# Kernel optimization log

Measured on AMD Instinct MI355X. Metric: run time of the kernel, lower is better.

Reference implementation:

```python
import jax, jax.numpy as jnp
import numpy as np

N_NODES = 100000
N_EDGES = 1600000
N_REL = 2
IN_CH, HID_CH, OUT_CH = 128, 128, 64


def setup_inputs() -> dict:
    key = jax.random.key(0)
    ks = jax.random.split(key, 8)
    x = jax.random.normal(ks[0], (N_NODES, IN_CH), dtype=jnp.float32)
    edge_index = jax.random.randint(ks[1], (2, N_EDGES), 0, N_NODES, dtype=jnp.int64)
    edge_type = jax.random.randint(ks[2], (N_EDGES,), 0, N_REL, dtype=jnp.int64)
    s1 = 1.0 / np.sqrt(IN_CH)
    s2 = 1.0 / np.sqrt(HID_CH)
    W1_rel = jax.random.normal(ks[3], (N_REL, IN_CH, HID_CH), dtype=jnp.float32) * s1
    W1_root = jax.random.normal(ks[4], (IN_CH, HID_CH), dtype=jnp.float32) * s1
    b1 = jnp.zeros((HID_CH,), dtype=jnp.float32)
    W2_rel = jax.random.normal(ks[5], (N_REL, HID_CH, OUT_CH), dtype=jnp.float32) * s2
    W2_root = jax.random.normal(ks[6], (HID_CH, OUT_CH), dtype=jnp.float32) * s2
    b2 = jnp.zeros((OUT_CH,), dtype=jnp.float32)
    return {"x": x, "edge_index": edge_index, "edge_type": edge_type,
            "W1_rel": W1_rel, "W1_root": W1_root, "b1": b1,
            "W2_rel": W2_rel, "W2_root": W2_root, "b2": b2}


def rgcn_conv(x, edge_index, edge_type, W_rel, W_root, b):
    """Relational graph conv: root transform + per-relation gather/matmul/scatter-mean."""
    src, dst = edge_index[0], edge_index[1]
    N = x.shape[0]
    out = x @ W_root + b  # self/root term
    x_src = x[src]  # [E, in] gather once, reused across relations
    for r in range(W_rel.shape[0]):  # N_REL is small and fixed
        mask = (edge_type == r)
        msg = jnp.where(mask[:, None], x_src, 0.0) @ W_rel[r]  # [E, out]
        agg = jax.ops.segment_sum(msg, dst, num_segments=N)  # [N, out]
        cnt = jax.ops.segment_sum(mask.astype(x.dtype), dst, num_segments=N)
        out = out + agg / jnp.maximum(cnt, 1.0)[:, None]  # mean aggregation
    return out


def l2_normalize(x, eps=1e-12):
    nrm = jnp.sqrt(jnp.sum(x * x, axis=1, keepdims=True))
    return x / jnp.maximum(nrm, eps)


def reference(x, edge_index, edge_type, W1_rel, W1_root, b1, W2_rel, W2_root, b2):
    h = jax.nn.relu(rgcn_conv(x, edge_index, edge_type, W1_rel, W1_root, b1))
    out = rgcn_conv(h, edge_index, edge_type, W2_rel, W2_root, b2)
    return l2_normalize(out)
```

## Files before the change

kernel.cpp:

```cpp
#include <hip/hip_runtime.h>
#include <hip/hip_bf16.h>


typedef unsigned int uint;
typedef unsigned short ushort;
typedef __attribute__((ext_vector_type(8))) short short8;
typedef __attribute__((ext_vector_type(16))) float floatx16;
typedef __attribute__((ext_vector_type(2))) float f32x2;
typedef __attribute__((ext_vector_type(4))) float f32x4;
typedef __attribute__((ext_vector_type(4))) uint u32x4;

#define IN_CH  128
#define OUT_CH 64
#define SCAN_CHUNK 2048
#define EPB 8192
#define KPB 512
#define MAXBK 400

__device__ __forceinline__ ushort f2bf(float f) {
    uint u = __float_as_uint(f);
    u += 0x7FFF + ((u >> 16) & 1);
    return (ushort)(u >> 16);
}
__device__ __forceinline__ float bflo(uint u) { return __uint_as_float(u << 16); }
__device__ __forceinline__ float bfhi(uint u) { return __uint_as_float(u & 0xFFFF0000u); }


__global__ void k_scan_a(const int* __restrict__ deg, int* __restrict__ offs,
                         int* __restrict__ bsums, int n) {
    __shared__ int sdata[256];
    int b = blockIdx.x, t = threadIdx.x;
    int base = b * SCAN_CHUNK + t * 8;
    int v[8];
    int sum = 0;
#pragma unroll
    for (int i = 0; i < 8; i++) {
        int idx = base + i;
        int x = (idx < n) ? deg[idx] : 0;
        v[i] = sum;
        sum += x;
    }
    sdata[t] = sum;
    __syncthreads();
    for (int ofs = 1; ofs < 256; ofs <<= 1) {
        int val = sdata[t];
        int add = (t >= ofs) ? sdata[t - ofs] : 0;
        __syncthreads();
        sdata[t] = val + add;
        __syncthreads();
    }
    int texcl = (t == 0) ? 0 : sdata[t - 1];
    if (t == 255) bsums[b] = sdata[255];
#pragma unroll
    for (int i = 0; i < 8; i++) {
        int idx = base + i;
        if (idx < n) offs[idx] = texcl + v[i];
    }
}

__global__ void k_scan_b(int* __restrict__ bsums, int* __restrict__ offs, int nb, int n) {
    int t = threadIdx.x;
    if (nb <= 64) {
        int v = (t < nb) ? bsums[t] : 0;
        int s = v;
#pragma unroll
        for (int d = 1; d < 64; d <<= 1) {
            int u = __shfl_up(s, d, 64);
            if (t >= d) s += u;
        }
        if (t < nb) bsums[t] = s - v;
        if (t == 63) offs[n] = s;
    } else if (t == 0) {
        int run = 0;
        for (int b = 0; b < nb; b++) {
            int x = bsums[b];
            bsums[b] = run;
            run += x;
        }
        offs[n] = run;
    }
}

__global__ void k_part(const int* __restrict__ src, const int* __restrict__ dst,
                       const int* __restrict__ et, const int* __restrict__ basebb,
                       const int* __restrict__ bsums,
                       uint* __restrict__ stage, int E, int NBK, int NBLK) {
    __shared__ int cnt[MAXBK];
    __shared__ int basel[MAXBK];
    int tid = threadIdx.x, blk = blockIdx.x;
    for (int b = tid; b < NBK; b += 256) {
        cnt[b] = 0;
        int i = b * NBLK + blk;
        basel[b] = basebb[i] + bsums[i >> 11];
    }
    __syncthreads();
    int base = blk * EPB;
#pragma unroll 4
    for (int i = 0; i < EPB / 256; i++) {
        int e = base + i * 256 + tid;
        if (e < E) {
            int s = src[e];
            int key = 2 * dst[e] + et[e];
            int bk = key >> 9;
            int r = atomicAdd(&cnt[bk], 1);
            stage[basel[bk] + r] = ((uint)(key & 511) << 23) | (uint)s;
        }
    }
}

__global__ void k_fine(const uint* __restrict__ stage, const int* __restrict__ basebb,
                       const int* __restrict__ bsums,
                       int* __restrict__ offs, int* __restrict__ esrc,
                       int E, int NBK, int NBLK) {
    __shared__ int kcnt[KPB];
    __shared__ int kcur[KPB];
    __shared__ int ssum[256];
    int tid = threadIdx.x, b = blockIdx.x;
    int i0 = b * NBLK;
    int start = basebb[i0] + bsums[i0 >> 11];
    int endB = E;
    if (b != NBK - 1) {
        int i1 = (b + 1) * NBLK;
        endB = basebb[i1] + bsums[i1 >> 11];
    }
    int size = endB - start;

    kcnt[tid] = 0;
    kcnt[tid + 256] = 0;
    __syncthreads();
    for (int i = tid; i < size; i += 256)
        atomicAdd(&kcnt[stage[start + i] >> 23], 1);
    __syncthreads();
    int v0 = kcnt[2 * tid], v1 = kcnt[2 * tid + 1];
    ssum[tid] = v0 + v1;
    __syncthreads();
    for (int ofs = 1; ofs < 256; ofs <<= 1) {
        int val = ssum[tid];
        int add = (tid >= ofs) ? ssum[tid - ofs] : 0;
        __syncthreads();
        ssum[tid] = val + add;
        __syncthreads();
    }
    int texcl = (tid == 0) ? 0 : ssum[tid - 1];
    kcur[2 * tid] = texcl;
    kcur[2 * tid + 1] = texcl + v0;
    offs[(b << 9) + 2 * tid] = start + texcl + v0;
    offs[(b << 9) + 2 * tid + 1] = start + texcl + v0 + v1;
    __syncthreads();
    for (int i = tid; i < size; i += 256) {
        uint p = stage[start + i];
        int r = atomicAdd(&kcur[p >> 23], 1);
        esrc[start + r] = (int)(p & 0x7FFFFFu);
    }
}


__device__ __forceinline__ uint4 pack8(const ushort* o) {
    uint4 v;
    v.x = (uint)o[0] | ((uint)o[1] << 16);
    v.y = (uint)o[2] | ((uint)o[3] << 16);
    v.z = (uint)o[4] | ((uint)o[5] << 16);
    v.w = (uint)o[6] | ((uint)o[7] << 16);
    return v;
}

__global__ void k_pre(const int* __restrict__ dst, const int* __restrict__ et,
                      int* __restrict__ cntblk, int E, int NBK, int NBLK,
                      const float* __restrict__ x, uint4* __restrict__ xb, int n8,
                      const float* __restrict__ W1root, const float* __restrict__ W1rel,
                      const float* __restrict__ W2root, const float* __restrict__ W2rel,
                      uint4* __restrict__ Bpk1, uint4* __restrict__ Bpk2,
                      uint* __restrict__ xzero, uint* __restrict__ t2zero) {
    __shared__ int cnt[MAXBK];
    int tid = threadIdx.x;
    if ((int)blockIdx.x < NBLK) {
        int blk = blockIdx.x;
        for (int b = tid; b < NBK; b += 256) cnt[b] = 0;
        __syncthreads();
        int base = blk * EPB;
#pragma unroll 4
        for (int i = 0; i < EPB / 256; i++) {
            int e = base + i * 256 + tid;
            if (e < E) {
                int key = 2 * dst[e] + et[e];
                atomicAdd(&cnt[key >> 9], 1);
            }
        }
        __syncthreads();
        for (int b = tid; b < NBK; b += 256) cntblk[b * NBLK + blk] = cnt[b];
        return;
    }
    int bid = blockIdx.x - NBLK;
    if (bid < 40) {
        if (bid == 0) {
            if (tid < 64) xzero[tid] = 0;
            if (tid < 96) t2zero[tid] = 0;
        }
        int idx = bid * 256 + tid;
        ushort o[8];
        if (idx < 6144) {
            int id = idx;
            int ct = id >> 11;
            int c = id & 2047;
            int gn = c >> 9, s = (c >> 6) & 7, h = (c >> 5) & 1, n = c & 31;
            int k0 = s * 16 + h * 8;
            int col = gn * 32 + n;
            const float* W = (ct == 0) ? W1root : (W1rel + (size_t)(ct - 1) * 16384);
#pragma unroll
            for (int j = 0; j < 8; j++) o[j] = f2bf(W[(k0 + j) * 128 + col]);
            Bpk1[id] = pack8(o);
        } else {
            int id = idx - 6144;
            int ct = id >> 11;
            int c = id & 2047;
            int gn = c >> 9, s = (c >> 6) & 7, h = (c >> 5) & 1, n = c & 31;
            int k0 = s * 16 + h * 8;
            int colg = ct * 128 + gn * 32 + n;
#pragma unroll
            for (int j = 0; j < 8; j++) {
                float f = 0.f;
                if (colg < 64)       f = W2root[(k0 + j) * 64 + colg];
                else if (colg < 128) f = W2rel[(k0 + j) * 64 + (colg - 64)];
                else if (colg < 192) f = W2rel[8192 + (k0 + j) * 64 + (colg - 128)];
                o[j] = f2bf(f);
            }
            Bpk2[id] = pack8(o);
        }
    } else {
        int i = (bid - 40) * 256 + tid;
        if (i >= n8) return;
        const f32x4* xp = (const f32x4*)x;
        f32x4 f0 = __builtin_nontemporal_load(&xp[(size_t)i * 2]);
        f32x4 f1 = __builtin_nontemporal_load(&xp[(size_t)i * 2 + 1]);
        uint4 o;
        o.x = (uint)f2bf(f0.x) | ((uint)f2bf(f0.y) << 16);
        o.y = (uint)f2bf(f0.z) | ((uint)f2bf(f0.w) << 16);
        o.z = (uint)f2bf(f1.x) | ((uint)f2bf(f1.y) << 16);
        o.w = (uint)f2bf(f1.z) | ((uint)f2bf(f1.w) << 16);
        xb[i] = o;
    }
}


__global__ __launch_bounds__(256)
void k_agg(const int* __restrict__ offs, const int* __restrict__ esrc,
           const uint4* __restrict__ xb4, uint4* __restrict__ S4, int N) {
    int wid = (int)((blockIdx.x * 256L + threadIdx.x) >> 5);
    int l = threadIdx.x & 31;
    if (wid >= N) return;
    int q = l >> 4, c = l & 15;

    int beg0 = (wid == 0) ? 0 : offs[2 * wid - 1];
    int end0 = offs[2 * wid], end1 = offs[2 * wid + 1];

    uint4 o = make_uint4(0, 0, 0, 0);
#pragma unroll
    for (int r = 0; r < 2; r++) {
        int beg = r ? end0 : beg0;
        int end = r ? end1 : end0;
        f32x2 a0 = {0.f, 0.f}, a1 = {0.f, 0.f}, a2 = {0.f, 0.f}, a3 = {0.f, 0.f};
        for (int c0 = beg; c0 < end; c0 += 32) {
            int myid = (c0 + l < end) ? __builtin_nontemporal_load(&esrc[c0 + l]) : N;
            int m = min(32, end - c0);
            for (int eb = 0; eb < m; eb += 4) {
#pragma unroll
                for (int j = 0; j < 2; j++) {
                    int id = __shfl(myid, eb + 2 * j + q, 32);
                    uint4 v = xb4[(uint)id * 16u + (uint)c];
                    a0 += (f32x2){bflo(v.x), bfhi(v.x)};
                    a1 += (f32x2){bflo(v.y), bfhi(v.y)};
                    a2 += (f32x2){bflo(v.z), bfhi(v.z)};
                    a3 += (f32x2){bflo(v.w), bfhi(v.w)};
                }
            }
        }
        a0.x += __shfl_xor(a0.x, 16, 32); a0.y += __shfl_xor(a0.y, 16, 32);
        a1.x += __shfl_xor(a1.x, 16, 32); a1.y += __shfl_xor(a1.y, 16, 32);
        a2.x += __shfl_xor(a2.x, 16, 32); a2.y += __shfl_xor(a2.y, 16, 32);
        a3.x += __shfl_xor(a3.x, 16, 32); a3.y += __shfl_xor(a3.y, 16, 32);
        if (q == r) {
            float inv = (end > beg) ? 1.0f / (float)(end - beg) : 0.f;
            o.x = (uint)f2bf(a0.x * inv) | ((uint)f2bf(a0.y * inv) << 16);
            o.y = (uint)f2bf(a1.x * inv) | ((uint)f2bf(a1.y * inv) << 16);
            o.z = (uint)f2bf(a2.x * inv) | ((uint)f2bf(a2.y * inv) << 16);
            o.w = (uint)f2bf(a3.x * inv) | ((uint)f2bf(a3.y * inv) << 16);
        }
    }
    S4[(size_t)wid * 32 + q * 16 + c] = o;
}


__global__ __launch_bounds__(512)
void k_fused(const ushort* __restrict__ xb, const ushort* __restrict__ S1,
             const ushort* __restrict__ Bpk1, const float* __restrict__ b1,
             const ushort* __restrict__ Bpk2, ushort* __restrict__ Out, int N) {
    __shared__ ushort SH[40960];
    ushort* Alds = SH;
    ushort* Blds = SH + 16384;

    const int tid = threadIdx.x;
    const int lane = tid & 63;
    const int w = tid >> 6;
    const int wm = w & 3;
    const int wn = w >> 2;
    const int rowBase = blockIdx.x * 128;

    floatx16 acc[2] = {};

#pragma unroll
    for (int seg = 0; seg < 3; seg++) {
        const ushort* Ap = (seg == 0) ? xb : S1;
        const int stride = (seg == 0) ? 128 : 256;
        const int aoff = (seg == 2) ? 128 : 0;
        const uint4* Bsrc = (const uint4*)Bpk1 + seg * 2048;
#pragma unroll
        for (int i = 0; i < 4; i++) {
            int c = tid + i * 512;
            int m = c & 31, hh = (c >> 5) & 1, s = (c >> 6) & 7, g = c >> 9;
            int row = rowBase + g * 32 + m;
            if (row >= N) row = N - 1;
            int kc = s * 2 + hh;
            ((uint4*)Alds)[c] = *(const uint4*)(Ap + (size_t)row * stride + aoff + kc * 8);
            ((uint4*)Blds)[c] = Bsrc[c];
        }
        __syncthreads();
#pragma unroll
        for (int s = 0; s < 8; s++) {
            short8 a0 = *(const short8*)&Alds[((wm * 8 + s) * 64 + lane) * 8];
            short8 b0 = *(const short8*)&Blds[(((wn * 2 + 0) * 8 + s) * 64 + lane) * 8];
            short8 b1f = *(const short8*)&Blds[(((wn * 2 + 1) * 8 + s) * 64 + lane) * 8];
            acc[0] = __builtin_amdgcn_mfma_f32_32x32x16_bf16(a0, b0, acc[0], 0, 0, 0);
            acc[1] = __builtin_amdgcn_mfma_f32_32x32x16_bf16(a0, b1f, acc[1], 0, 0, 0);
        }
        __syncthreads();
    }

    {
        const int qr = 4 * (lane >> 5);
        const int cl = lane & 31;
#pragma unroll
        for (int nt = 0; nt < 2; nt++) {
            float bb = b1[wn * 64 + nt * 32 + cl];
            int col = wn * 64 + nt * 32 + cl;
            int kc = col >> 3, j = col & 7;
            int s = kc >> 1, hh = kc & 1;
            int base = ((wm * 8 + s) * 64 + hh * 32) * 8 + j;
#pragma unroll
            for (int reg = 0; reg < 16; reg++) {
                int rl = (reg & 3) + 8 * (reg >> 2) + qr;
                float v = fmaxf(acc[nt][reg] + bb, 0.f);
                Alds[base + rl * 8] = f2bf(v);
            }
        }
        const uint4* B2s = (const uint4*)Bpk2;
#pragma unroll
        for (int i = 0; i < 6; i++) {
            int c = tid + i * 512;
            ((uint4*)Blds)[c] = B2s[c];
        }
    }
    __syncthreads();

    floatx16 acc2[3] = {};
#pragma unroll
    for (int s = 0; s < 8; s++) {
        short8 a0 = *(const short8*)&Alds[((wm * 8 + s) * 64 + lane) * 8];
        short8 b0 = *(const short8*)&Blds[(((wn * 3 + 0) * 8 + s) * 64 + lane) * 8];
        short8 b1v = *(const short8*)&Blds[(((wn * 3 + 1) * 8 + s) * 64 + lane) * 8];
        short8 b2v = *(const short8*)&Blds[(((wn * 3 + 2) * 8 + s) * 64 + lane) * 8];
        acc2[0] = __builtin_amdgcn_mfma_f32_32x32x16_bf16(a0, b0, acc2[0], 0, 0, 0);
        acc2[1] = __builtin_amdgcn_mfma_f32_32x32x16_bf16(a0, b1v, acc2[1], 0, 0, 0);
        acc2[2] = __builtin_amdgcn_mfma_f32_32x32x16_bf16(a0, b2v, acc2[2], 0, 0, 0);
    }
    __syncthreads();

    ushort* Clds = SH;
    {
        const int qr = 4 * (lane >> 5);
        const int cl = lane & 31;
#pragma unroll
        for (int nt = 0; nt < 3; nt++) {
#pragma unroll
            for (int reg = 0; reg < 16; reg++) {
                int rl = (reg & 3) + 8 * (reg >> 2) + qr;
                Clds[(wm * 32 + rl) * 200 + wn * 96 + nt * 32 + cl] =
                    f2bf(acc2[nt][reg]);
            }
        }
    }
    __syncthreads();

    int r = tid >> 2, q4 = tid & 3;
    int grow = rowBase + r;
    if (grow < N) {
#pragma unroll
        for (int k = 0; k < 6; k++) {
            int c0 = q4 * 48 + k * 8;
            uint4 v = *(const uint4*)&Clds[r * 200 + c0];
            *(uint4*)(Out + (size_t)grow * 192 + c0) = v;
        }
    }
}


__global__ __launch_bounds__(256)
void k_final(const ushort* __restrict__ T2, const float* __restrict__ b2,
             const int* __restrict__ offs, const int* __restrict__ esrc,
             float* __restrict__ out, int N) {
    int wid = (int)((blockIdx.x * 256L + threadIdx.x) >> 3);
    int c = threadIdx.x & 7;
    if (wid >= N) return;
    const uint4* Tb = (const uint4*)T2;

    int beg0 = (wid == 0) ? 0 : offs[2 * wid - 1];
    int end0 = offs[2 * wid], end1 = offs[2 * wid + 1];

    f32x2 t0 = {0.f, 0.f}, t1 = {0.f, 0.f}, t2v = {0.f, 0.f}, t3v = {0.f, 0.f};
#pragma unroll
    for (int r = 0; r < 2; r++) {
        int beg = r ? end0 : beg0;
        int end = r ? end1 : end0;
        if (end > beg) {
            f32x2 a0 = {0.f, 0.f}, a1 = {0.f, 0.f}, a2 = {0.f, 0.f}, a3 = {0.f, 0.f};
            uint bc = 8u + 8u * (uint)r + (uint)c;
            for (int c0 = beg; c0 < end; c0 += 8) {
                int myid = (c0 + c < end) ? __builtin_nontemporal_load(&esrc[c0 + c]) : N;
                int m = min(8, end - c0);
                for (int eb = 0; eb < m; eb += 4) {
                    uint4 v[4];
#pragma unroll
                    for (int j = 0; j < 4; j++) {
                        int id = __shfl(myid, eb + j, 8);
                        v[j] = Tb[(uint)id * 24u + bc];
                    }
#pragma unroll
                    for (int j = 0; j < 4; j++) {
                        a0 += (f32x2){bflo(v[j].x), bfhi(v[j].x)};
                        a1 += (f32x2){bflo(v[j].y), bfhi(v[j].y)};
                        a2 += (f32x2){bflo(v[j].z), bfhi(v[j].z)};
                        a3 += (f32x2){bflo(v[j].w), bfhi(v[j].w)};
                    }
                }
            }
            float inv = 1.0f / (float)(end - beg);
            t0 += a0 * inv; t1 += a1 * inv; t2v += a2 * inv; t3v += a3 * inv;
        }
    }
    uint4 ru = Tb[(uint)wid * 24u + (uint)c];
    float4 bbA = *(const float4*)(b2 + 8 * c);
    float4 bbB = *(const float4*)(b2 + 8 * c + 4);
    float v0 = bflo(ru.x) + bbA.x + t0.x;
    float v1 = bfhi(ru.x) + bbA.y + t0.y;
    float v2 = bflo(ru.y) + bbA.z + t1.x;
    float v3 = bfhi(ru.y) + bbA.w + t1.y;
    float v4 = bflo(ru.z) + bbB.x + t2v.x;
    float v5 = bfhi(ru.z) + bbB.y + t2v.y;
    float v6 = bflo(ru.w) + bbB.z + t3v.x;
    float v7 = bfhi(ru.w) + bbB.w + t3v.y;
    float sq = v0 * v0 + v1 * v1 + v2 * v2 + v3 * v3
             + v4 * v4 + v5 * v5 + v6 * v6 + v7 * v7;
#pragma unroll
    for (int d = 1; d <= 4; d <<= 1) sq += __shfl_xor(sq, d, 8);
    float rn = 1.0f / fmaxf(sqrtf(sq), 1e-12f);
    f32x4 oA = {v0 * rn, v1 * rn, v2 * rn, v3 * rn};
    f32x4 oB = {v4 * rn, v5 * rn, v6 * rn, v7 * rn};
    f32x4* op = (f32x4*)(out + (size_t)wid * 64 + 8 * c);
    __builtin_nontemporal_store(oA, op);
    __builtin_nontemporal_store(oB, op + 1);
}


extern "C" void kernel_launch(void* const* d_in, const int* in_sizes, int n_in,
                              void* d_out, int out_size, void* d_ws, size_t ws_size,
                              hipStream_t stream) {
    const float* x      = (const float*)d_in[0];
    const int*   ei     = (const int*)d_in[1];
    const int*   etype  = (const int*)d_in[2];
    const float* W1rel  = (const float*)d_in[3];
    const float* W1root = (const float*)d_in[4];
    const float* b1     = (const float*)d_in[5];
    const float* W2rel  = (const float*)d_in[6];
    const float* W2root = (const float*)d_in[7];
    const float* b2     = (const float*)d_in[8];
    float* out = (float*)d_out;

    const int N = in_sizes[0] / IN_CH;
    const int E = in_sizes[2];
    const int NKEY = 2 * N;
    const int NBK  = (NKEY + KPB - 1) / KPB;
    const int NBLK = (E + EPB - 1) / EPB;
    const int NSC  = NBK * NBLK;

    const int* src = ei;
    const int* dst = ei + E;

    char* base = (char*)d_ws;
    size_t off = 0;
    auto carve = [&](size_t bytes) -> void* {
        void* p = base + off;
        off = (off + bytes + 511) & ~(size_t)511;
        return p;
    };
    ushort* xb    = (ushort*)carve((size_t)(N + 1) * 128 * sizeof(ushort));
    ushort* S1    = (ushort*)carve((size_t)N * 256 * sizeof(ushort));
    ushort* t2    = (ushort*)carve((size_t)(N + 1) * 192 * sizeof(ushort));
    int*    esrc  = (int*)carve((size_t)E * sizeof(int));
    uint*   stage = (uint*)carve((size_t)E * sizeof(uint));
    int*    offs  = (int*)carve((size_t)NBK * KPB * sizeof(int));
    int*    cntblk= (int*)carve((size_t)NSC * sizeof(int));
    int*    basebb= (int*)carve((size_t)(NSC + 1) * sizeof(int));
    int     NB    = (NSC + SCAN_CHUNK - 1) / SCAN_CHUNK;
    int*    bsums = (int*)carve((size_t)NB * sizeof(int));
    uint4*  Bpk1  = (uint4*)carve(6144 * sizeof(uint4));
    uint4*  Bpk2  = (uint4*)carve(4096 * sizeof(uint4));
    (void)ws_size; (void)n_in; (void)out_size;

    int n8 = N * 16;
    int preBlocks = NBLK + 40 + (n8 + 255) / 256;

    k_pre<<<preBlocks, 256, 0, stream>>>(dst, etype, cntblk, E, NBK, NBLK,
                                         x, (uint4*)xb, n8,
                                         W1root, W1rel, W2root, W2rel,
                                         Bpk1, Bpk2,
                                         (uint*)(xb + (size_t)N * 128),
                                         (uint*)(t2 + (size_t)N * 192));

    k_scan_a<<<NB, 256, 0, stream>>>(cntblk, basebb, bsums, NSC);
    k_scan_b<<<1, 64, 0, stream>>>(bsums, basebb, NB, NSC);
    k_part<<<NBLK, 256, 0, stream>>>(src, dst, etype, basebb, bsums, stage, E, NBK, NBLK);
    k_fine<<<NBK, 256, 0, stream>>>(stage, basebb, bsums, offs, esrc, E, NBK, NBLK);

    int rowTiles = (N + 127) / 128;
    int aggBlocks = (N + 7) / 8;
    int finBlocks = (N + 31) / 32;

    k_agg<<<aggBlocks, 256, 0, stream>>>(offs, esrc, (const uint4*)xb, (uint4*)S1, N);
    k_fused<<<rowTiles, 512, 0, stream>>>(xb, S1, (const ushort*)Bpk1, b1,
                                          (const ushort*)Bpk2, t2, N);

    k_final<<<finBlocks, 256, 0, stream>>>(t2, b2, offs, esrc, out, N);
}
```

Baseline: 310.4 us.

## Fuse neighbor mean aggregation into the first-layer MFMA kernel via LDS

Removes the separate aggregation kernel and its S1 intermediate buffer. Each block of the fused GEMM kernel now gathers and averages neighbor features per relation for its 128 rows, writing the bf16 means straight into the LDS A tile before the relation's MFMA. This avoids writing and re-reading the aggregated features through global memory and drops one launch, but the latency-bound gather now runs with far fewer, larger blocks and serialized row processing per wave group.

```diff
diff --git a/kernel.cpp b/kernel.cpp
--- a/kernel.cpp
+++ b/kernel.cpp
@@ -242,56 +242,9 @@
 }
 
 
-__global__ __launch_bounds__(256)
-void k_agg(const int* __restrict__ offs, const int* __restrict__ esrc,
-           const uint4* __restrict__ xb4, uint4* __restrict__ S4, int N) {
-    int wid = (int)((blockIdx.x * 256L + threadIdx.x) >> 5);
-    int l = threadIdx.x & 31;
-    if (wid >= N) return;
-    int q = l >> 4, c = l & 15;
-
-    int beg0 = (wid == 0) ? 0 : offs[2 * wid - 1];
-    int end0 = offs[2 * wid], end1 = offs[2 * wid + 1];
-
-    uint4 o = make_uint4(0, 0, 0, 0);
-#pragma unroll
-    for (int r = 0; r < 2; r++) {
-        int beg = r ? end0 : beg0;
-        int end = r ? end1 : end0;
-        f32x2 a0 = {0.f, 0.f}, a1 = {0.f, 0.f}, a2 = {0.f, 0.f}, a3 = {0.f, 0.f};
-        for (int c0 = beg; c0 < end; c0 += 32) {
-            int myid = (c0 + l < end) ? __builtin_nontemporal_load(&esrc[c0 + l]) : N;
-            int m = min(32, end - c0);
-            for (int eb = 0; eb < m; eb += 4) {
-#pragma unroll
-                for (int j = 0; j < 2; j++) {
-                    int id = __shfl(myid, eb + 2 * j + q, 32);
-                    uint4 v = xb4[(uint)id * 16u + (uint)c];
-                    a0 += (f32x2){bflo(v.x), bfhi(v.x)};
-                    a1 += (f32x2){bflo(v.y), bfhi(v.y)};
-                    a2 += (f32x2){bflo(v.z), bfhi(v.z)};
-                    a3 += (f32x2){bflo(v.w), bfhi(v.w)};
-                }
-            }
-        }
-        a0.x += __shfl_xor(a0.x, 16, 32); a0.y += __shfl_xor(a0.y, 16, 32);
-        a1.x += __shfl_xor(a1.x, 16, 32); a1.y += __shfl_xor(a1.y, 16, 32);
-        a2.x += __shfl_xor(a2.x, 16, 32); a2.y += __shfl_xor(a2.y, 16, 32);
-        a3.x += __shfl_xor(a3.x, 16, 32); a3.y += __shfl_xor(a3.y, 16, 32);
-        if (q == r) {
-            float inv = (end > beg) ? 1.0f / (float)(end - beg) : 0.f;
-            o.x = (uint)f2bf(a0.x * inv) | ((uint)f2bf(a0.y * inv) << 16);
-            o.y = (uint)f2bf(a1.x * inv) | ((uint)f2bf(a1.y * inv) << 16);
-            o.z = (uint)f2bf(a2.x * inv) | ((uint)f2bf(a2.y * inv) << 16);
-            o.w = (uint)f2bf(a3.x * inv) | ((uint)f2bf(a3.y * inv) << 16);
-        }
-    }
-    S4[(size_t)wid * 32 + q * 16 + c] = o;
-}
-
-
-__global__ __launch_bounds__(512)
-void k_fused(const ushort* __restrict__ xb, const ushort* __restrict__ S1,
+__global__ __launch_bounds__(512, 4)
+void k_fused(const ushort* __restrict__ xb,
+             const int* __restrict__ offs, const int* __restrict__ esrc,
              const ushort* __restrict__ Bpk1, const float* __restrict__ b1,
              const ushort* __restrict__ Bpk2, ushort* __restrict__ Out, int N) {
     __shared__ ushort SH[40960];
@@ -304,15 +257,12 @@
     const int wm = w & 3;
     const int wn = w >> 2;
     const int rowBase = blockIdx.x * 128;
+    const uint4* xb4 = (const uint4*)xb;
 
     floatx16 acc[2] = {};
 
-#pragma unroll
-    for (int seg = 0; seg < 3; seg++) {
-        const ushort* Ap = (seg == 0) ? xb : S1;
-        const int stride = (seg == 0) ? 128 : 256;
-        const int aoff = (seg == 2) ? 128 : 0;
-        const uint4* Bsrc = (const uint4*)Bpk1 + seg * 2048;
+    {
+        const uint4* Bsrc = (const uint4*)Bpk1;
 #pragma unroll
         for (int i = 0; i < 4; i++) {
             int c = tid + i * 512;
@@ -320,8 +270,70 @@
             int row = rowBase + g * 32 + m;
             if (row >= N) row = N - 1;
             int kc = s * 2 + hh;
-            ((uint4*)Alds)[c] = *(const uint4*)(Ap + (size_t)row * stride + aoff + kc * 8);
+            ((uint4*)Alds)[c] = *(const uint4*)(xb + (size_t)row * 128 + kc * 8);
             ((uint4*)Blds)[c] = Bsrc[c];
+        }
+        __syncthreads();
+#pragma unroll
+        for (int s = 0; s < 8; s++) {
+            short8 a0 = *(const short8*)&Alds[((wm * 8 + s) * 64 + lane) * 8];
+            short8 b0 = *(const short8*)&Blds[(((wn * 2 + 0) * 8 + s) * 64 + lane) * 8];
+            short8 b1f = *(const short8*)&Blds[(((wn * 2 + 1) * 8 + s) * 64 + lane) * 8];
+            acc[0] = __builtin_amdgcn_mfma_f32_32x32x16_bf16(a0, b0, acc[0], 0, 0, 0);
+            acc[1] = __builtin_amdgcn_mfma_f32_32x32x16_bf16(a0, b1f, acc[1], 0, 0, 0);
+        }
+        __syncthreads();
+    }
+
+    const int l = tid & 31;
+    const int grp = tid >> 5;
+    const int q = l >> 4, ch = l & 15;
+#pragma unroll
+    for (int rel = 0; rel < 2; rel++) {
+        const uint4* Bsrc = (const uint4*)Bpk1 + (rel + 1) * 2048;
+#pragma unroll
+        for (int i = 0; i < 4; i++) {
+            int c = tid + i * 512;
+            ((uint4*)Blds)[c] = Bsrc[c];
+        }
+        for (int p = 0; p < 8; p++) {
+            int rloc = grp * 8 + p;
+            int wid = rowBase + rloc;
+            if (wid < N) {
+                int key = 2 * wid + rel;
+                int beg = (key == 0) ? 0 : offs[key - 1];
+                int end = offs[key];
+                f32x2 a0 = {0.f, 0.f}, a1 = {0.f, 0.f}, a2 = {0.f, 0.f}, a3 = {0.f, 0.f};
+                for (int c0 = beg; c0 < end; c0 += 32) {
+                    int myid = (c0 + l < end) ? __builtin_nontemporal_load(&esrc[c0 + l]) : N;
+                    int m = min(32, end - c0);
+                    for (int eb = 0; eb < m; eb += 4) {
+#pragma unroll
+                        for (int j = 0; j < 2; j++) {
+                            int id = __shfl(myid, eb + 2 * j + q, 32);
+                            uint4 v = xb4[(uint)id * 16u + (uint)ch];
+                            a0 += (f32x2){bflo(v.x), bfhi(v.x)};
+                            a1 += (f32x2){bflo(v.y), bfhi(v.y)};
+                            a2 += (f32x2){bflo(v.z), bfhi(v.z)};
+                            a3 += (f32x2){bflo(v.w), bfhi(v.w)};
+                        }
+                    }
+                }
+                a0.x += __shfl_xor(a0.x, 16, 32); a0.y += __shfl_xor(a0.y, 16, 32);
+                a1.x += __shfl_xor(a1.x, 16, 32); a1.y += __shfl_xor(a1.y, 16, 32);
+                a2.x += __shfl_xor(a2.x, 16, 32); a2.y += __shfl_xor(a2.y, 16, 32);
+                a3.x += __shfl_xor(a3.x, 16, 32); a3.y += __shfl_xor(a3.y, 16, 32);
+                if (q == 0) {
+                    float inv = (end > beg) ? 1.0f / (float)(end - beg) : 0.f;
+                    uint4 o;
+                    o.x = (uint)f2bf(a0.x * inv) | ((uint)f2bf(a0.y * inv) << 16);
+                    o.y = (uint)f2bf(a1.x * inv) | ((uint)f2bf(a1.y * inv) << 16);
+                    o.z = (uint)f2bf(a2.x * inv) | ((uint)f2bf(a2.y * inv) << 16);
+                    o.w = (uint)f2bf(a3.x * inv) | ((uint)f2bf(a3.y * inv) << 16);
+                    int g = rloc >> 5, m2 = rloc & 31, s = ch >> 1, hh = ch & 1;
+                    ((uint4*)Alds)[(g * 8 + s) * 64 + hh * 32 + m2] = o;
+                }
+            }
         }
         __syncthreads();
 #pragma unroll
@@ -502,7 +514,6 @@
         return p;
     };
     ushort* xb    = (ushort*)carve((size_t)(N + 1) * 128 * sizeof(ushort));
-    ushort* S1    = (ushort*)carve((size_t)N * 256 * sizeof(ushort));
     ushort* t2    = (ushort*)carve((size_t)(N + 1) * 192 * sizeof(ushort));
     int*    esrc  = (int*)carve((size_t)E * sizeof(int));
     uint*   stage = (uint*)carve((size_t)E * sizeof(uint));
@@ -531,11 +542,10 @@
     k_fine<<<NBK, 256, 0, stream>>>(stage, basebb, bsums, offs, esrc, E, NBK, NBLK);
 
     int rowTiles = (N + 127) / 128;
-    int aggBlocks = (N + 7) / 8;
     int finBlocks = (N + 31) / 32;
 
-    k_agg<<<aggBlocks, 256, 0, stream>>>(offs, esrc, (const uint4*)xb, (uint4*)S1, N);
-    k_fused<<<rowTiles, 512, 0, stream>>>(xb, S1, (const ushort*)Bpk1, b1,
+    k_fused<<<rowTiles, 512, 0, stream>>>(xb, offs, esrc,
+                                          (const ushort*)Bpk1, b1,
                                           (const ushort*)Bpk2, t2, N);
 
     k_final<<<finBlocks, 256, 0, stream>>>(t2, b2, offs, esrc, out, N);
```

After: 314.3 us. About the same (+1.3%).

## Replace two-level bucket partition sort with global atomic counting sort

Applied to the files above, without the earlier changes.

Drops the staged partition scheme (per-block bucket histograms, coarse partition, then fine per-bucket sort in shared memory). It now builds a direct per-key histogram with global atomics, scans it, and scatters source indices using atomic position fetch on the key offsets. After the scatter each offset holds the end of its key, which matches the end-offset convention the earlier code used. This removes the stage buffer and two kernels, but adds a memset, an extra scan fix-up kernel and millions of global returning atomics with random writes. Edge order within each key also becomes nondeterministic.

```diff
diff --git a/kernel.cpp b/kernel.cpp
--- a/kernel.cpp
+++ b/kernel.cpp
@@ -12,10 +12,8 @@
 
 #define IN_CH  128
 #define OUT_CH 64
-#define SCAN_CHUNK 2048
+#define SCAN_CHUNK 4096
 #define EPB 8192
-#define KPB 512
-#define MAXBK 400
 
 __device__ __forceinline__ ushort f2bf(float f) {
     uint u = __float_as_uint(f);
@@ -30,11 +28,11 @@
                          int* __restrict__ bsums, int n) {
     __shared__ int sdata[256];
     int b = blockIdx.x, t = threadIdx.x;
-    int base = b * SCAN_CHUNK + t * 8;
-    int v[8];
+    int base = b * SCAN_CHUNK + t * 16;
+    int v[16];
     int sum = 0;
 #pragma unroll
-    for (int i = 0; i < 8; i++) {
+    for (int i = 0; i < 16; i++) {
         int idx = base + i;
         int x = (idx < n) ? deg[idx] : 0;
         v[i] = sum;
@@ -52,7 +50,7 @@
     int texcl = (t == 0) ? 0 : sdata[t - 1];
     if (t == 255) bsums[b] = sdata[255];
 #pragma unroll
-    for (int i = 0; i < 8; i++) {
+    for (int i = 0; i < 16; i++) {
         int idx = base + i;
         if (idx < n) offs[idx] = texcl + v[i];
     }
@@ -81,76 +79,19 @@
     }
 }
 
-__global__ void k_part(const int* __restrict__ src, const int* __restrict__ dst,
-                       const int* __restrict__ et, const int* __restrict__ basebb,
-                       const int* __restrict__ bsums,
-                       uint* __restrict__ stage, int E, int NBK, int NBLK) {
-    __shared__ int cnt[MAXBK];
-    __shared__ int basel[MAXBK];
-    int tid = threadIdx.x, blk = blockIdx.x;
-    for (int b = tid; b < NBK; b += 256) {
-        cnt[b] = 0;
-        int i = b * NBLK + blk;
-        basel[b] = basebb[i] + bsums[i >> 11];
-    }
-    __syncthreads();
-    int base = blk * EPB;
-#pragma unroll 4
-    for (int i = 0; i < EPB / 256; i++) {
-        int e = base + i * 256 + tid;
-        if (e < E) {
-            int s = src[e];
-            int key = 2 * dst[e] + et[e];
-            int bk = key >> 9;
-            int r = atomicAdd(&cnt[bk], 1);
-            stage[basel[bk] + r] = ((uint)(key & 511) << 23) | (uint)s;
-        }
-    }
-}
-
-__global__ void k_fine(const uint* __restrict__ stage, const int* __restrict__ basebb,
-                       const int* __restrict__ bsums,
-                       int* __restrict__ offs, int* __restrict__ esrc,
-                       int E, int NBK, int NBLK) {
-    __shared__ int kcnt[KPB];
-    __shared__ int kcur[KPB];
-    __shared__ int ssum[256];
-    int tid = threadIdx.x, b = blockIdx.x;
-    int i0 = b * NBLK;
-    int start = basebb[i0] + bsums[i0 >> 11];
-    int endB = E;
-    if (b != NBK - 1) {
-        int i1 = (b + 1) * NBLK;
-        endB = basebb[i1] + bsums[i1 >> 11];
-    }
-    int size = endB - start;
-
-    kcnt[tid] = 0;
-    kcnt[tid + 256] = 0;
-    __syncthreads();
-    for (int i = tid; i < size; i += 256)
-        atomicAdd(&kcnt[stage[start + i] >> 23], 1);
-    __syncthreads();
-    int v0 = kcnt[2 * tid], v1 = kcnt[2 * tid + 1];
-    ssum[tid] = v0 + v1;
-    __syncthreads();
-    for (int ofs = 1; ofs < 256; ofs <<= 1) {
-        int val = ssum[tid];
-        int add = (tid >= ofs) ? ssum[tid - ofs] : 0;
-        __syncthreads();
-        ssum[tid] = val + add;
-        __syncthreads();
-    }
-    int texcl = (tid == 0) ? 0 : ssum[tid - 1];
-    kcur[2 * tid] = texcl;
-    kcur[2 * tid + 1] = texcl + v0;
-    offs[(b << 9) + 2 * tid] = start + texcl + v0;
-    offs[(b << 9) + 2 * tid + 1] = start + texcl + v0 + v1;
-    __syncthreads();
-    for (int i = tid; i < size; i += 256) {
-        uint p = stage[start + i];
-        int r = atomicAdd(&kcur[p >> 23], 1);
-        esrc[start + r] = (int)(p & 0x7FFFFFu);
+__global__ void k_scan_c(int* __restrict__ offs, const int* __restrict__ bsums, int n) {
+    int i = blockIdx.x * blockDim.x + threadIdx.x;
+    if (i < n) offs[i] += bsums[i >> 12];
+}
+
+__global__ void k_scatter(const int* __restrict__ src, const int* __restrict__ dst,
+                          const int* __restrict__ et, int* __restrict__ koffs,
+                          int* __restrict__ esrc, int E) {
+    int e = blockIdx.x * 256 + threadIdx.x;
+    if (e < E) {
+        int key = 2 * dst[e] + et[e];
+        int pos = atomicAdd(&koffs[key], 1);
+        esrc[pos] = src[e];
     }
 }
 
@@ -165,29 +106,23 @@
 }
 
 __global__ void k_pre(const int* __restrict__ dst, const int* __restrict__ et,
-                      int* __restrict__ cntblk, int E, int NBK, int NBLK,
+                      int* __restrict__ kcnt, int E, int NBLK,
                       const float* __restrict__ x, uint4* __restrict__ xb, int n8,
                       const float* __restrict__ W1root, const float* __restrict__ W1rel,
                       const float* __restrict__ W2root, const float* __restrict__ W2rel,
                       uint4* __restrict__ Bpk1, uint4* __restrict__ Bpk2,
                       uint* __restrict__ xzero, uint* __restrict__ t2zero) {
-    __shared__ int cnt[MAXBK];
     int tid = threadIdx.x;
     if ((int)blockIdx.x < NBLK) {
-        int blk = blockIdx.x;
-        for (int b = tid; b < NBK; b += 256) cnt[b] = 0;
-        __syncthreads();
-        int base = blk * EPB;
+        int base = blockIdx.x * EPB;
 #pragma unroll 4
         for (int i = 0; i < EPB / 256; i++) {
             int e = base + i * 256 + tid;
             if (e < E) {
                 int key = 2 * dst[e] + et[e];
-                atomicAdd(&cnt[key >> 9], 1);
-            }
-        }
-        __syncthreads();
-        for (int b = tid; b < NBK; b += 256) cntblk[b * NBLK + blk] = cnt[b];
+                atomicAdd(&kcnt[key], 1);
+            }
+        }
         return;
     }
     int bid = blockIdx.x - NBLK;
@@ -487,9 +422,7 @@
     const int N = in_sizes[0] / IN_CH;
     const int E = in_sizes[2];
     const int NKEY = 2 * N;
-    const int NBK  = (NKEY + KPB - 1) / KPB;
     const int NBLK = (E + EPB - 1) / EPB;
-    const int NSC  = NBK * NBLK;
 
     const int* src = ei;
     const int* dst = ei + E;
@@ -505,11 +438,9 @@
     ushort* S1    = (ushort*)carve((size_t)N * 256 * sizeof(ushort));
     ushort* t2    = (ushort*)carve((size_t)(N + 1) * 192 * sizeof(ushort));
     int*    esrc  = (int*)carve((size_t)E * sizeof(int));
-    uint*   stage = (uint*)carve((size_t)E * sizeof(uint));
-    int*    offs  = (int*)carve((size_t)NBK * KPB * sizeof(int));
-    int*    cntblk= (int*)carve((size_t)NSC * sizeof(int));
-    int*    basebb= (int*)carve((size_t)(NSC + 1) * sizeof(int));
-    int     NB    = (NSC + SCAN_CHUNK - 1) / SCAN_CHUNK;
+    int*    kcnt  = (int*)carve((size_t)NKEY * sizeof(int));
+    int*    koffs = (int*)carve((size_t)(NKEY + 1) * sizeof(int));
+    int     NB    = (NKEY + SCAN_CHUNK - 1) / SCAN_CHUNK;
     int*    bsums = (int*)carve((size_t)NB * sizeof(int));
     uint4*  Bpk1  = (uint4*)carve(6144 * sizeof(uint4));
     uint4*  Bpk2  = (uint4*)carve(4096 * sizeof(uint4));
@@ -518,25 +449,27 @@
     int n8 = N * 16;
     int preBlocks = NBLK + 40 + (n8 + 255) / 256;
 
-    k_pre<<<preBlocks, 256, 0, stream>>>(dst, etype, cntblk, E, NBK, NBLK,
+    hipMemsetAsync(kcnt, 0, (size_t)NKEY * sizeof(int), stream);
+
+    k_pre<<<preBlocks, 256, 0, stream>>>(dst, etype, kcnt, E, NBLK,
                                          x, (uint4*)xb, n8,
                                          W1root, W1rel, W2root, W2rel,
                                          Bpk1, Bpk2,
                                          (uint*)(xb + (size_t)N * 128),
                                          (uint*)(t2 + (size_t)N * 192));
 
-    k_scan_a<<<NB, 256, 0, stream>>>(cntblk, basebb, bsums, NSC);
-    k_scan_b<<<1, 64, 0, stream>>>(bsums, basebb, NB, NSC);
-    k_part<<<NBLK, 256, 0, stream>>>(src, dst, etype, basebb, bsums, stage, E, NBK, NBLK);
-    k_fine<<<NBK, 256, 0, stream>>>(stage, basebb, bsums, offs, esrc, E, NBK, NBLK);
+    k_scan_a<<<NB, 256, 0, stream>>>(kcnt, koffs, bsums, NKEY);
+    k_scan_b<<<1, 64, 0, stream>>>(bsums, koffs, NB, NKEY);
+    k_scan_c<<<(NKEY + 255) / 256, 256, 0, stream>>>(koffs, bsums, NKEY);
+    k_scatter<<<(E + 255) / 256, 256, 0, stream>>>(src, dst, etype, koffs, esrc, E);
 
     int rowTiles = (N + 127) / 128;
     int aggBlocks = (N + 7) / 8;
     int finBlocks = (N + 31) / 32;
 
-    k_agg<<<aggBlocks, 256, 0, stream>>>(offs, esrc, (const uint4*)xb, (uint4*)S1, N);
+    k_agg<<<aggBlocks, 256, 0, stream>>>(koffs, esrc, (const uint4*)xb, (uint4*)S1, N);
     k_fused<<<rowTiles, 512, 0, stream>>>(xb, S1, (const ushort*)Bpk1, b1,
                                           (const ushort*)Bpk2, t2, N);
 
-    k_final<<<finBlocks, 256, 0, stream>>>(t2, b2, offs, esrc, out, N);
-}
+    k_final<<<finBlocks, 256, 0, stream>>>(t2, b2, koffs, esrc, out, N);
+}
```

After: 425.8 us. +37.2%, slower.
